# Kernel optimization log

Measured on AMD Instinct MI355X. Metric: run time of the kernel, lower is better.

The kernel has to match this reference:

```python
import jax, jax.numpy as jnp
import numpy as np

N_HEAD = 16

def setup_inputs() -> dict:
    key = jax.random.key(0)
    ks = jax.random.split(key, 5)
    B, T, C = 4, 2048, 1024
    x = jax.random.normal(ks[0], (B, T, C), dtype=jnp.float32)
    # Linear params (torch nn.Linear: y = x @ W.T + b), init scaled like default
    s = 1.0 / np.sqrt(C)
    W_attn = jax.random.uniform(ks[1], (3 * C, C), dtype=jnp.float32, minval=-s, maxval=s)
    b_attn = jax.random.uniform(ks[2], (3 * C,), dtype=jnp.float32, minval=-s, maxval=s)
    W_proj = jax.random.uniform(ks[3], (C, C), dtype=jnp.float32, minval=-s, maxval=s)
    b_proj = jax.random.uniform(ks[4], (C,), dtype=jnp.float32, minval=-s, maxval=s)
    return {"x": x, "W_attn": W_attn, "b_attn": b_attn, "W_proj": W_proj, "b_proj": b_proj}

def reference(x, W_attn, b_attn, W_proj, b_proj):
    B, T, C = x.shape
    H = N_HEAD
    D = C // H
    qkv = jnp.einsum('btc,oc->bto', x, W_attn) + b_attn  # [B,T,3C]
    q, k, v = jnp.split(qkv, 3, axis=2)
    # [B,H,T,D]
    q = q.reshape(B, T, H, D).transpose(0, 2, 1, 3)
    k = k.reshape(B, T, H, D).transpose(0, 2, 1, 3)
    v = v.reshape(B, T, H, D).transpose(0, 2, 1, 3)
    att = jnp.einsum('bhtd,bhsd->bhts', q, k) * (1.0 / np.sqrt(D))  # [B,H,T,T]
    causal = jnp.tril(jnp.ones((T, T), dtype=bool))
    att = jnp.where(causal, att, -jnp.inf)
    att = jax.nn.softmax(att, axis=-1)
    y = jnp.einsum('bhts,bhsd->bhtd', att, v)  # [B,H,T,D]
    y = y.transpose(0, 2, 1, 3).reshape(B, T, C)
    return jnp.einsum('btc,oc->bto', y, W_proj) + b_proj
```

## Files before the change

kernel.cpp:

```cpp
#include <hip/hip_runtime.h>
#include <stdint.h>

typedef unsigned short u16;
typedef __attribute__((ext_vector_type(8))) short short8;
typedef __attribute__((ext_vector_type(4))) float float4v;

#define MFMA16(a, b, c) __builtin_amdgcn_mfma_f32_16x16x32_bf16((a), (b), (c), 0, 0, 0)

#define Q_SCALE 0.18033688011112042f

__device__ __forceinline__ int swz(int row, int col) {
  return row * 64 + (col & 7) + ((((col >> 3) ^ row) & 7) << 3);
}

__device__ __forceinline__ u16 f2b(float f) {
  union { float f; unsigned u; } x; x.f = f;
  unsigned r = x.u + 0x7fffu + ((x.u >> 16) & 1u);
  return (u16)(r >> 16);
}

__device__ __forceinline__ unsigned pack2(float a, float b) {
  return (unsigned)f2b(a) | ((unsigned)f2b(b) << 16);
}

__device__ __forceinline__ void load_lds_16(const void* g, void* l) {
  __builtin_amdgcn_global_load_lds((__attribute__((address_space(1))) void*)g,
                                   (__attribute__((address_space(3))) void*)l,
                                   16, 0, 0);
}

__global__ __launch_bounds__(256) void cvt_bf16(const float* __restrict__ in,
                                                u16* __restrict__ out, int n8) {
  int i = blockIdx.x * 256 + threadIdx.x;
  if (i >= n8) return;
  const float4* p = (const float4*)in + (size_t)i * 2;
  float4 a = p[0], b = p[1];
  uint4 w;
  w.x = pack2(a.x, a.y);
  w.y = pack2(a.z, a.w);
  w.z = pack2(b.x, b.y);
  w.w = pack2(b.z, b.w);
  *(uint4*)&out[(size_t)i * 8] = w;
}

__global__ __launch_bounds__(256) void transpose_v(const u16* __restrict__ V,
                                                   u16* __restrict__ Vt) {
  __shared__ u16 tile[64][72];
  const int bh = blockIdx.y;
  const int t0 = blockIdx.x * 64;
  const int tid = threadIdx.x;
  const int r = tid >> 3, c = (tid & 7) * 8;
#pragma unroll
  for (int h = 0; h < 2; ++h) {
    uint4 v = *(const uint4*)&V[((size_t)bh * 2048 + t0 + r + h * 32) * 64 + c];
    const u16* p = (const u16*)&v;
#pragma unroll
    for (int j = 0; j < 8; ++j) tile[c + j][r + h * 32] = p[j];
  }
  __syncthreads();
#pragma unroll
  for (int h = 0; h < 2; ++h) {
    uint4 w;
    u16* p = (u16*)&w;
#pragma unroll
    for (int j = 0; j < 8; ++j) p[j] = tile[r + h * 32][c + j];
    *(uint4*)&Vt[((size_t)bh * 64 + r + h * 32) * 2048 + t0 + c] = w;
  }
}

template <bool QKV_OUT>
__global__ __launch_bounds__(256) void gemm_bt(const u16* __restrict__ A,
                                               const u16* __restrict__ B,
                                               const float* __restrict__ bias,
                                               float* __restrict__ Cf,
                                               u16* __restrict__ QKV,
                                               int M, int N, int K) {
  __shared__ __align__(16) u16 As[128 * 64];
  __shared__ __align__(16) u16 Bs[128 * 64];
  const int tid = threadIdx.x;
  const int lane = tid & 63;
  const int wave = tid >> 6;
  const int quad = lane >> 4;
  const int l15 = lane & 15;
  const int bm0 = blockIdx.y * 128;
  const int bn0 = blockIdx.x * 128;
  const int wm = (wave & 1) * 64;
  const int wn = (wave >> 1) * 64;

  float4v acc[4][4];
#pragma unroll
  for (int i = 0; i < 4; ++i)
#pragma unroll
    for (int j = 0; j < 4; ++j) acc[i][j] = (float4v){0.f, 0.f, 0.f, 0.f};

  const int srow = wave * 32 + (lane >> 3);
  const int scol = ((lane & 7) ^ ((lane >> 3) & 7)) * 8;

  for (int k0 = 0; k0 < K; k0 += 64) {
#pragma unroll
    for (int s = 0; s < 4; ++s) {
      const int r = s * 8;
      load_lds_16(&A[(size_t)(bm0 + srow + r) * K + k0 + scol], &As[(wave * 32 + r) * 64]);
      load_lds_16(&B[(size_t)(bn0 + srow + r) * K + k0 + scol], &Bs[(wave * 32 + r) * 64]);
    }
    __builtin_amdgcn_s_waitcnt(0);
    __syncthreads();
#pragma unroll
    for (int ks = 0; ks < 2; ++ks) {
      short8 af[4], bf[4];
#pragma unroll
      for (int t = 0; t < 4; ++t) {
        af[t] = *(const short8*)&As[swz(wm + t * 16 + l15, ks * 32 + quad * 8)];
        bf[t] = *(const short8*)&Bs[swz(wn + t * 16 + l15, ks * 32 + quad * 8)];
      }
#pragma unroll
      for (int mt = 0; mt < 4; ++mt)
#pragma unroll
        for (int nt = 0; nt < 4; ++nt)
          acc[mt][nt] = MFMA16(af[mt], bf[nt], acc[mt][nt]);
    }
    __syncthreads();
  }

#pragma unroll
  for (int mt = 0; mt < 4; ++mt) {
    const int row0 = bm0 + wm + mt * 16 + quad * 4;
#pragma unroll
    for (int nt = 0; nt < 4; ++nt) {
      const int col = bn0 + wn + nt * 16 + l15;
      const float bs = bias[col];
      if constexpr (QKV_OUT) {
        const int which = col >> 10;
        const int rem = col & 1023;
        const int h = rem >> 6;
        const int d = rem & 63;
        const float sc = (which == 0) ? Q_SCALE : 1.0f;
#pragma unroll
        for (int i = 0; i < 4; ++i) {
          const int t = row0 + i;
          const int b = t >> 11;
          const int tt = t & 2047;
          QKV[(size_t)which * 8388608 +
              ((size_t)(b * 16 + h) * 2048 + tt) * 64 + d] = f2b((acc[mt][nt][i] + bs) * sc);
        }
      } else {
#pragma unroll
        for (int i = 0; i < 4; ++i)
          Cf[(size_t)(row0 + i) * N + col] = acc[mt][nt][i] + bs;
      }
    }
  }
}

__global__ __launch_bounds__(256) void attn_kernel(const u16* __restrict__ QKV,
                                                   const u16* __restrict__ Vt_g,
                                                   u16* __restrict__ Y) {
  const int bx = blockIdx.x;
  const int bh = blockIdx.y;
  const int b = bh >> 4, h = bh & 15;
  const int tid = threadIdx.x;
  const int lane = tid & 63;
  const int wave = tid >> 6;
  const int quad = lane >> 4;
  const int l15 = lane & 15;
  const int qt[2] = {bx, 31 - bx};

  const u16* Qg = QKV + (size_t)bh * 2048 * 64;
  const u16* Kg = QKV + 8388608 + (size_t)bh * 2048 * 64;
  const u16* Vg = Vt_g + (size_t)bh * 64 * 2048;

  __shared__ __align__(16) u16 Ks[3][64 * 64];

  short8 qf[2][2];
#pragma unroll
  for (int u = 0; u < 2; ++u)
#pragma unroll
    for (int ks = 0; ks < 2; ++ks)
      qf[u][ks] = *(const short8*)&Qg[(size_t)(qt[u] * 64 + wave * 16 + l15) * 64 + ks * 32 + quad * 8];

  float4v o[2][4];
  float4v rsacc[2];
#pragma unroll
  for (int u = 0; u < 2; ++u) {
    rsacc[u] = (float4v){0.f, 0.f, 0.f, 0.f};
#pragma unroll
    for (int i = 0; i < 4; ++i) o[u][i] = (float4v){0.f, 0.f, 0.f, 0.f};
  }

  const short8 ones8 = {0x3F80, 0x3F80, 0x3F80, 0x3F80, 0x3F80, 0x3F80, 0x3F80, 0x3F80};

  const int r8 = lane >> 3;
  const int c8 = ((lane & 7) ^ r8) * 8;
  auto stageK = [&](int st_, int bufi) {
    const int sb = st_ * 64;
#pragma unroll
    for (int p = 0; p < 2; ++p) {
      const int c = wave * 2 + p;
      load_lds_16(&Kg[(size_t)(sb + c * 8 + r8) * 64 + c8], &Ks[bufi][c * 512]);
    }
  };

  short8 vf[8];
  auto load_vf = [&](int st_) {
    const u16* VgS = Vg + st_ * 64;
#pragma unroll
    for (int ks = 0; ks < 2; ++ks)
#pragma unroll
      for (int dt = 0; dt < 4; ++dt)
        vf[ks * 4 + dt] = *(const short8*)&VgS[(size_t)(dt * 16 + l15) * 2048 + ks * 32 + quad * 8];
    asm volatile("" ::: "memory");
  };

  const int last = qt[1];
  stageK(0, 0);
  stageK(1, 1);
  load_vf(0);
  asm volatile("s_waitcnt vmcnt(10)" ::: "memory");
  __builtin_amdgcn_s_barrier();

  int cur = 0;
  for (int st = 0; st <= last; ++st) {
    const bool pf = (st + 2 <= last);
    if (pf) {
      int nb = cur + 2; if (nb >= 3) nb -= 3;
      stageK(st + 2, nb);
    }
    const bool both = (st <= qt[0]);

    float4v s[2][4];
#pragma unroll
    for (int u = 0; u < 2; ++u)
#pragma unroll
      for (int nt = 0; nt < 4; ++nt) s[u][nt] = (float4v){0.f, 0.f, 0.f, 0.f};
    __builtin_amdgcn_s_setprio(1);
#pragma unroll
    for (int ks = 0; ks < 2; ++ks)
#pragma unroll
      for (int nt = 0; nt < 4; ++nt) {
        const short8 kf = *(const short8*)&Ks[cur][swz(nt * 16 + l15, ks * 32 + quad * 8)];
        s[1][nt] = MFMA16(kf, qf[1][ks], s[1][nt]);
        if (both) s[0][nt] = MFMA16(kf, qf[0][ks], s[0][nt]);
      }
    __builtin_amdgcn_s_setprio(0);

    short8 af[2][2];
#pragma unroll
    for (int u = 0; u < 2; ++u) {
      if (u == 0 && !both) continue;

      if (st == qt[u]) {
        const int qrow = wave * 16 + l15;
        const int kb = quad * 4;
#pragma unroll
        for (int nt = 0; nt < 4; ++nt)
#pragma unroll
          for (int i = 0; i < 4; ++i)
            if (kb + nt * 16 + i > qrow) s[u][nt][i] = -1e30f;
      }

      unsigned pkx[4], pky[4];
#pragma unroll
      for (int nt = 0; nt < 4; ++nt) {
        const float p0 = __builtin_amdgcn_exp2f(s[u][nt][0]);
        const float p1 = __builtin_amdgcn_exp2f(s[u][nt][1]);
        const float p2 = __builtin_amdgcn_exp2f(s[u][nt][2]);
        const float p3 = __builtin_amdgcn_exp2f(s[u][nt][3]);
        pkx[nt] = pack2(p0, p1);
        pky[nt] = pack2(p2, p3);
      }

#pragma unroll
      for (int ks = 0; ks < 2; ++ks) {
        unsigned ax = pkx[2 * ks], bx2 = pkx[2 * ks + 1];
        unsigned ay = pky[2 * ks], by2 = pky[2 * ks + 1];
        asm("v_permlane32_swap_b32 %0, %1" : "+v"(ax), "+v"(bx2));
        asm("v_permlane16_swap_b32 %0, %1" : "+v"(ax), "+v"(bx2));
        asm("v_permlane32_swap_b32 %0, %1" : "+v"(ay), "+v"(by2));
        asm("v_permlane16_swap_b32 %0, %1" : "+v"(ay), "+v"(by2));
        uint4 w;
        w.x = ax; w.y = ay; w.z = bx2; w.w = by2;
        af[u][ks] = *(const short8*)&w;
        rsacc[u] = MFMA16(af[u][ks], ones8, rsacc[u]);
      }
    }

    if (pf) asm volatile("s_waitcnt vmcnt(2)" ::: "memory");
    else    asm volatile("s_waitcnt vmcnt(0)" ::: "memory");

    __builtin_amdgcn_s_setprio(1);
#pragma unroll
    for (int ks = 0; ks < 2; ++ks)
#pragma unroll
      for (int dt = 0; dt < 4; ++dt) {
        o[1][dt] = MFMA16(af[1][ks], vf[ks * 4 + dt], o[1][dt]);
        if (both) o[0][dt] = MFMA16(af[0][ks], vf[ks * 4 + dt], o[0][dt]);
      }
    __builtin_amdgcn_s_setprio(0);

    if (st < last) load_vf(st + 1);
    __builtin_amdgcn_s_barrier();

    ++cur; if (cur >= 3) cur = 0;
  }

#pragma unroll
  for (int u = 0; u < 2; ++u) {
    float linv[4];
#pragma unroll
    for (int i = 0; i < 4; ++i) linv[i] = 1.0f / rsacc[u][i];
#pragma unroll
    for (int dt = 0; dt < 4; ++dt)
#pragma unroll
      for (int i = 0; i < 4; ++i) {
        const float v = o[u][dt][i] * linv[i];
        const int t = qt[u] * 64 + wave * 16 + quad * 4 + i;
        Y[((size_t)b * 2048 + t) * 1024 + h * 64 + dt * 16 + l15] = f2b(v);
      }
  }
}

extern "C" void kernel_launch(void* const* d_in, const int* in_sizes, int n_in,
                              void* d_out, int out_size, void* d_ws, size_t ws_size,
                              hipStream_t stream) {
  const float* x  = (const float*)d_in[0];
  const float* Wa = (const float*)d_in[1];
  const float* ba = (const float*)d_in[2];
  const float* Wp = (const float*)d_in[3];
  const float* bp = (const float*)d_in[4];
  float* out = (float*)d_out;

  u16* xb  = (u16*)d_ws;
  u16* Wab = xb + 8388608;
  u16* Wpb = Wab + 3145728;
  u16* qkv = Wpb + 1048576;
  u16* y   = xb;
  u16* vt  = (u16*)d_out;

  cvt_bf16<<<4096, 256, 0, stream>>>(x, xb, 1048576);
  cvt_bf16<<<1536, 256, 0, stream>>>(Wa, Wab, 393216);
  cvt_bf16<<<512, 256, 0, stream>>>(Wp, Wpb, 131072);

  gemm_bt<true><<<dim3(24, 64), 256, 0, stream>>>(xb, Wab, ba, nullptr, qkv, 8192, 3072, 1024);
  transpose_v<<<dim3(32, 64), 256, 0, stream>>>(qkv + 16777216, vt);
  attn_kernel<<<dim3(16, 64), 256, 0, stream>>>(qkv, vt, y);
  gemm_bt<false><<<dim3(8, 64), 256, 0, stream>>>(y, Wpb, bp, out, nullptr, 8192, 1024, 1024);
}
```

Baseline: 331.7 us.

## Stage V tiles through double-buffered LDS and remap block IDs for locality

The attention kernel now stages V tiles into a double-buffered, swizzled LDS buffer using async global-to-LDS loads, instead of loading V fragments straight into registers. The vmcnt waits move to the end of each iteration. Both the GEMM and attention kernels also remap the workgroup index with an 8-way interleave, aiming for better cache locality across compute dies. This frees VGPRs and lets V prefetch overlap compute, at the cost of extra LDS traffic and reads, and the wait counts now have to match the new load ordering.

```diff
diff --git a/kernel.cpp b/kernel.cpp
--- a/kernel.cpp
+++ b/kernel.cpp
@@ -82,8 +82,13 @@
   const int wave = tid >> 6;
   const int quad = lane >> 4;
   const int l15 = lane & 15;
-  const int bm0 = blockIdx.y * 128;
-  const int bn0 = blockIdx.x * 128;
+
+  const int nwg = gridDim.x * gridDim.y;
+  int id = blockIdx.y * gridDim.x + blockIdx.x;
+  id = (id & 7) * (nwg >> 3) + (id >> 3);
+  const int bm0 = (id / gridDim.x) * 128;
+  const int bn0 = (id % gridDim.x) * 128;
+
   const int wm = (wave & 1) * 64;
   const int wn = (wave >> 1) * 64;
 
@@ -155,8 +160,10 @@
 __global__ __launch_bounds__(256) void attn_kernel(const u16* __restrict__ QKV,
                                                    const u16* __restrict__ Vt_g,
                                                    u16* __restrict__ Y) {
-  const int bx = blockIdx.x;
-  const int bh = blockIdx.y;
+  int id = blockIdx.y * 16 + blockIdx.x;
+  id = (id & 7) * 128 + (id >> 3);
+  const int bx = id & 15;
+  const int bh = id >> 4;
   const int b = bh >> 4, h = bh & 15;
   const int tid = threadIdx.x;
   const int lane = tid & 63;
@@ -170,6 +177,7 @@
   const u16* Vg = Vt_g + (size_t)bh * 64 * 2048;
 
   __shared__ __align__(16) u16 Ks[3][64 * 64];
+  __shared__ __align__(16) u16 Vt[2][64 * 64];
 
   short8 qf[2][2];
 #pragma unroll
@@ -192,36 +200,33 @@
   const int r8 = lane >> 3;
   const int c8 = ((lane & 7) ^ r8) * 8;
   auto stageK = [&](int st_, int bufi) {
-    const int sb = st_ * 64;
 #pragma unroll
     for (int p = 0; p < 2; ++p) {
       const int c = wave * 2 + p;
-      load_lds_16(&Kg[(size_t)(sb + c * 8 + r8) * 64 + c8], &Ks[bufi][c * 512]);
+      load_lds_16(&Kg[(size_t)(st_ * 64 + c * 8 + r8) * 64 + c8], &Ks[bufi][c * 512]);
     }
   };
-
-  short8 vf[8];
-  auto load_vf = [&](int st_) {
-    const u16* VgS = Vg + st_ * 64;
-#pragma unroll
-    for (int ks = 0; ks < 2; ++ks)
-#pragma unroll
-      for (int dt = 0; dt < 4; ++dt)
-        vf[ks * 4 + dt] = *(const short8*)&VgS[(size_t)(dt * 16 + l15) * 2048 + ks * 32 + quad * 8];
-    asm volatile("" ::: "memory");
+  auto stageV = [&](int st_, int bufi) {
+#pragma unroll
+    for (int p = 0; p < 2; ++p) {
+      const int c = wave * 2 + p;
+      load_lds_16(&Vg[(size_t)(c * 8 + r8) * 2048 + st_ * 64 + c8], &Vt[bufi][c * 512]);
+    }
   };
 
   const int last = qt[1];
+  stageV(0, 0);
   stageK(0, 0);
   stageK(1, 1);
-  load_vf(0);
-  asm volatile("s_waitcnt vmcnt(10)" ::: "memory");
+  asm volatile("s_waitcnt vmcnt(2)" ::: "memory");
   __builtin_amdgcn_s_barrier();
 
   int cur = 0;
   for (int st = 0; st <= last; ++st) {
-    const bool pf = (st + 2 <= last);
-    if (pf) {
+    const int vcur = st & 1;
+    if (st + 1 <= last) stageV(st + 1, vcur ^ 1);
+    const bool pfk = (st + 2 <= last);
+    if (pfk) {
       int nb = cur + 2; if (nb >= 3) nb -= 3;
       stageK(st + 2, nb);
     }
@@ -284,20 +289,19 @@
       }
     }
 
-    if (pf) asm volatile("s_waitcnt vmcnt(2)" ::: "memory");
-    else    asm volatile("s_waitcnt vmcnt(0)" ::: "memory");
-
     __builtin_amdgcn_s_setprio(1);
 #pragma unroll
     for (int ks = 0; ks < 2; ++ks)
 #pragma unroll
       for (int dt = 0; dt < 4; ++dt) {
-        o[1][dt] = MFMA16(af[1][ks], vf[ks * 4 + dt], o[1][dt]);
-        if (both) o[0][dt] = MFMA16(af[0][ks], vf[ks * 4 + dt], o[0][dt]);
+        const short8 vf = *(const short8*)&Vt[vcur][swz(dt * 16 + l15, ks * 32 + quad * 8)];
+        o[1][dt] = MFMA16(af[1][ks], vf, o[1][dt]);
+        if (both) o[0][dt] = MFMA16(af[0][ks], vf, o[0][dt]);
       }
     __builtin_amdgcn_s_setprio(0);
 
-    if (st < last) load_vf(st + 1);
+    if (pfk) asm volatile("s_waitcnt vmcnt(2)" ::: "memory");
+    else     asm volatile("s_waitcnt vmcnt(0)" ::: "memory");
     __builtin_amdgcn_s_barrier();
 
     ++cur; if (cur >= 3) cur = 0;
```

Result: faster. 286.2 us (-13.7%).
